# Performance work log

Measured on AMD Instinct MI355X. Metric: run time of the kernel, lower is better.

## Reference

```python
import jax, jax.numpy as jnp
import numpy as np

N = 100000   # points
C = 64       # in_planes
OUT = 64     # out_planes (== mid_planes)
S = 8        # share_planes
NS = 16      # nsample
EPS = 1e-5


def setup_inputs() -> dict:
    key = jax.random.key(0)
    ks = iter(jax.random.split(key, 40))
    rn = lambda shape, scale=1.0: jax.random.normal(next(ks), shape, jnp.float32) * scale

    inp = {
        'point': rn((N, 3)),
        'feat': rn((N, C)),
        'idx': jax.random.randint(next(ks), (N, NS), 0, N, jnp.int64),
        # linear_q / linear_k / linear_v
        'Wq': rn((C, OUT), C ** -0.5), 'bq': jnp.zeros((OUT,), jnp.float32),
        'Wk': rn((C, OUT), C ** -0.5), 'bk': jnp.zeros((OUT,), jnp.float32),
        'Wv': rn((C, OUT), C ** -0.5), 'bv': jnp.zeros((OUT,), jnp.float32),
        # linear_p: Dense(3) -> BN -> ReLU -> Dense(OUT)
        'p_W1': rn((3, 3), 3 ** -0.5), 'p_b1': rn((3,), 0.02),
        'p_g1': 1.0 + rn((3,), 0.02), 'p_be1': rn((3,), 0.02),
        'p_m1': rn((3,), 0.02), 'p_v1': 1.0 + 0.1 * jax.random.uniform(next(ks), (3,), jnp.float32),
        'p_W2': rn((3, OUT), 3 ** -0.5), 'p_b2': rn((OUT,), 0.02),
        # linear_w: BN -> ReLU -> Dense(OUT//S) -> BN -> ReLU -> Dense(OUT//S)
        'w_g1': 1.0 + rn((OUT,), 0.02), 'w_be1': rn((OUT,), 0.02),
        'w_m1': rn((OUT,), 0.02), 'w_v1': 1.0 + 0.1 * jax.random.uniform(next(ks), (OUT,), jnp.float32),
        'w_W1': rn((OUT, OUT // S), OUT ** -0.5), 'w_b1': rn((OUT // S,), 0.02),
        'w_g2': 1.0 + rn((OUT // S,), 0.02), 'w_be2': rn((OUT // S,), 0.02),
        'w_m2': rn((OUT // S,), 0.02), 'w_v2': 1.0 + 0.1 * jax.random.uniform(next(ks), (OUT // S,), jnp.float32),
        'w_W2': rn((OUT // S, OUT // S), (OUT // S) ** -0.5), 'w_b2': rn((OUT // S,), 0.02),
    }
    return inp


def _bn(x, g, b, m, v):  # inference-mode batchnorm over last axis
    return g * (x - m) * jax.lax.rsqrt(v + EPS) + b


def reference(point, feat, idx, Wq, bq, Wk, bk, Wv, bv,
              p_W1, p_b1, p_g1, p_be1, p_m1, p_v1, p_W2, p_b2,
              w_g1, w_be1, w_m1, w_v1, w_W1, w_b1,
              w_g2, w_be2, w_m2, w_v2, w_W2, w_b2):
    fq = feat @ Wq + bq                      # (n, out)
    fk = feat @ Wk + bk
    fv = feat @ Wv + bv

    # queryandgroup: KNN gather (idx precomputed)
    gx = point[idx] - point[:, None, :]      # (n, ns, 3) relative coords
    gk = fk[idx]                             # (n, ns, out)
    gv = fv[idx]                             # (n, ns, out)

    # linear_p position encoding MLP
    pr = jnp.maximum(_bn(gx @ p_W1 + p_b1, p_g1, p_be1, p_m1, p_v1), 0.0)
    pr = pr @ p_W2 + p_b2                    # (n, ns, out)

    # vector attention logits; out_planes//mid_planes == 1 so reduce_sum is identity
    w = gk - fq[:, None, :] + pr             # (n, ns, out)
    w = jnp.maximum(_bn(w, w_g1, w_be1, w_m1, w_v1), 0.0)
    w = w @ w_W1 + w_b1
    w = jnp.maximum(_bn(w, w_g2, w_be2, w_m2, w_v2), 0.0)
    w = w @ w_W2 + w_b2                      # (n, ns, out//s)
    w = jax.nn.softmax(w, axis=1)            # softmax over neighbors

    a = (gv + pr).reshape(-1, NS, S, OUT // S)         # (n, ns, s, out//s)
    out = jnp.sum(a * w[:, :, None, :], axis=1)        # (n, s, out//s)
    return out.reshape(-1, OUT)
```

## Files before the change

### kernel.cpp

```cpp
#include <hip/hip_runtime.h>
#include <hip/hip_fp16.h>

typedef unsigned short ushort_t;
typedef unsigned int u32;
typedef short short8 __attribute__((ext_vector_type(8)));
typedef float f32x2 __attribute__((ext_vector_type(2)));
typedef float f32x4 __attribute__((ext_vector_type(4)));
typedef u32 u32x4 __attribute__((ext_vector_type(4)));
typedef __fp16 h16x2 __attribute__((ext_vector_type(2)));
typedef _Float16 h16v8 __attribute__((ext_vector_type(8)));

#define N_PTS 100000
#define NSAMP 16
#define LOG2E 1.44269504088896340736f

__device__ __forceinline__ ushort_t f2h(float f) {
    __fp16 h = (__fp16)f; return __builtin_bit_cast(ushort_t, h);
}
__device__ __forceinline__ u32 pk2h(float lo, float hi) {
    return __builtin_bit_cast(u32, __builtin_amdgcn_cvt_pkrtz(lo, hi));
}
__device__ __forceinline__ float h2f_lo(u32 p) { return __low2float(__builtin_bit_cast(__half2, p)); }
__device__ __forceinline__ float h2f_hi(u32 p) { return __high2float(__builtin_bit_cast(__half2, p)); }
__device__ __forceinline__ u32 hadd2u(u32 a, u32 b) {
    return __builtin_bit_cast(u32, __hadd2(__builtin_bit_cast(__half2, a), __builtin_bit_cast(__half2, b)));
}
__device__ __forceinline__ u32 hsub2u(u32 a, u32 b) {
    return __builtin_bit_cast(u32, __hsub2(__builtin_bit_cast(__half2, a), __builtin_bit_cast(__half2, b)));
}
__device__ __forceinline__ u32 hmul2u(u32 a, u32 b) {
    return __builtin_bit_cast(u32, __hmul2(__builtin_bit_cast(__half2, a), __builtin_bit_cast(__half2, b)));
}
__device__ __forceinline__ u32 hmax2u(u32 a, u32 b) {
    u32 r; asm("v_pk_max_f16 %0, %1, %2" : "=v"(r) : "v"(a), "v"(b)); return r;
}
__device__ __forceinline__ float rfl(float x) {
    return __builtin_bit_cast(float, (int)__builtin_amdgcn_readfirstlane(__builtin_bit_cast(int, x)));
}
__device__ __forceinline__ f32x4 mfma16(u32x4 a, short8 b, f32x4 c) {
    return __builtin_amdgcn_mfma_f32_16x16x32_f16(
        __builtin_bit_cast(h16v8, a), __builtin_bit_cast(h16v8, b), c, 0, 0, 0);
}

__global__ __launch_bounds__(256, 4) void qkv_kernel(
    const float* __restrict__ feat,
    const float* __restrict__ Wq, const float* __restrict__ bq,
    const float* __restrict__ Wk, const float* __restrict__ bk,
    const float* __restrict__ Wv, const float* __restrict__ bv,
    ushort_t* __restrict__ qkv)
{
    const int tid  = threadIdx.x;
    const int lane = tid & 63;
    const int wid  = tid >> 6;
    const int jl   = lane & 15;
    const int g    = lane >> 4;

    const float* Ws[3] = {Wq, Wk, Wv};
    const float* bs[3] = {bq, bk, bv};

    short8 bfrag[3][4][2];
    float  bias[3][4];
#pragma unroll
    for (int m = 0; m < 3; m++)
#pragma unroll
        for (int cb = 0; cb < 4; cb++) {
#pragma unroll
            for (int h = 0; h < 2; h++) {
                short8 f;
#pragma unroll
                for (int e = 0; e < 8; e++)
                    f[e] = (short)f2h(Ws[m][(h * 32 + g * 8 + e) * 64 + cb * 16 + jl]);
                bfrag[m][cb][h] = f;
            }
            bias[m][cb] = bs[m][cb * 16 + jl];
        }

    const int nwaves = gridDim.x * (blockDim.x >> 6);
    const int gw     = blockIdx.x * (blockDim.x >> 6) + wid;
    const int ntiles = N_PTS / 16;

    for (int t = gw; t < ntiles; t += nwaves) {
        const int i0 = t * 16;
        const float* arow = feat + (i0 + jl) * 64;
        const f32x4 a00 = *(const f32x4*)(arow + g * 8);
        const f32x4 a01 = *(const f32x4*)(arow + g * 8 + 4);
        const f32x4 a10 = *(const f32x4*)(arow + 32 + g * 8);
        const f32x4 a11 = *(const f32x4*)(arow + 32 + g * 8 + 4);
        u32x4 ap0, ap1;
#pragma unroll
        for (int e = 0; e < 2; e++) {
            ap0[e]     = pk2h(a00[2 * e], a00[2 * e + 1]);
            ap0[2 + e] = pk2h(a01[2 * e], a01[2 * e + 1]);
            ap1[e]     = pk2h(a10[2 * e], a10[2 * e + 1]);
            ap1[2 + e] = pk2h(a11[2 * e], a11[2 * e + 1]);
        }
#pragma unroll
        for (int m = 0; m < 3; m++)
#pragma unroll
            for (int cb = 0; cb < 4; cb++) {
                f32x4 acc = {0.f, 0.f, 0.f, 0.f};
                acc = mfma16(ap0, bfrag[m][cb][0], acc);
                acc = mfma16(ap1, bfrag[m][cb][1], acc);
#pragma unroll
                for (int r = 0; r < 4; r++) {
                    const int row = i0 + g * 4 + r;
                    qkv[row * 192 + m * 64 + cb * 16 + jl] = f2h(acc[r] + bias[m][cb]);
                }
            }
    }
}

__global__ __launch_bounds__(256, 2) void attn_kernel(
    const float* __restrict__ point, const int* __restrict__ idx,
    const ushort_t* __restrict__ qkv,
    const float* pW1, const float* pb1, const float* pg1, const float* pbe1,
    const float* pm1, const float* pv1, const float* pW2, const float* pb2,
    const float* wg1, const float* wbe1, const float* wm1, const float* wv1,
    const float* wW1, const float* wb1, const float* wg2, const float* wbe2,
    const float* wm2, const float* wv2, const float* wW2, const float* wb2,
    float* __restrict__ out)
{
    __shared__ float lds[4][720];

    const int tid  = threadIdx.x;
    const int lane = tid & 63;
    const int wid  = tid >> 6;
    const int jl   = lane & 15;
    const int g    = lane >> 4;

    int zp = 0;
#pragma unroll
    for (int k = 0; k < 16; k++) zp |= idx[2 * k + 1];
    const bool idx64 = (zp == 0);

    float A1s[3][3], c1[3];
#pragma unroll
    for (int u = 0; u < 3; u++) {
        const float s = pg1[u] * rsqrtf(pv1[u] + 1e-5f);
        c1[u] = rfl((pb1[u] - pm1[u]) * s + pbe1[u]);
#pragma unroll
        for (int t = 0; t < 3; t++) A1s[t][u] = rfl(pW1[t * 3 + u] * s);
    }
    h16x2 w01[2][8];
    float w2c[2][8], pb2cc[2][8];
    u32 bwh[2][4];
#pragma unroll
    for (int h = 0; h < 2; h++) {
#pragma unroll
        for (int e = 0; e < 8; e++) {
            const int c = h * 32 + g * 8 + e;
            w01[h][e]   = __builtin_amdgcn_cvt_pkrtz(pW2[0 * 64 + c], pW2[1 * 64 + c]);
            w2c[h][e]   = pW2[2 * 64 + c];
            pb2cc[h][e] = pb2[c];
        }
#pragma unroll
        for (int q = 0; q < 4; q++) {
            const int c0 = h * 32 + g * 8 + 2 * q;
            const float s0 = wg1[c0] * rsqrtf(wv1[c0] + 1e-5f);
            const float s1 = wg1[c0 + 1] * rsqrtf(wv1[c0 + 1] + 1e-5f);
            bwh[h][q] = pk2h(wbe1[c0] / s0 - wm1[c0], wbe1[c0 + 1] / s1 - wm1[c0 + 1]);
        }
    }
    short8 w1f[2];
#pragma unroll
    for (int h = 0; h < 2; h++)
#pragma unroll
        for (int e = 0; e < 8; e++) {
            const int c = h * 32 + g * 8 + e;
            const float s = wg1[c] * rsqrtf(wv1[c] + 1e-5f);
            w1f[h][e] = (jl < 8) ? (short)f2h(wW1[c * 8 + jl] * s) : (short)0;
        }
    const float s2o  = (jl < 8) ? wg2[jl] * rsqrtf(wv2[jl] + 1e-5f) : 1.f;
    const float b2nd = (jl < 8) ? (wb1[jl] + wbe2[jl] / s2o - wm2[jl]) : 0.f;
    short8 w2f;
#pragma unroll
    for (int e = 0; e < 8; e++) {
        const float s2e = wg2[e] * rsqrtf(wv2[e] + 1e-5f);
        w2f[e] = (g == 0 && jl < 8) ? (short)f2h(wW2[e * 8 + jl] * s2e * LOG2E) : (short)0;
    }
    const float b2o = (jl < 8) ? wb2[jl] * LOG2E : 0.f;

    float* l12 = &lds[wid][0];
    u32*   tlu = (u32*)&lds[wid][192];

    const int nwaves = gridDim.x * (blockDim.x >> 6);
    const int gw     = blockIdx.x * (blockDim.x >> 6) + wid;

    const char* qb  = (const char*)qkv;
    const u32   gsl = (u32)g * 16u;

    for (int i = gw; i < N_PTS; i += nwaves) {
        const int nb = idx64 ? idx[(i * NSAMP + jl) * 2] : idx[i * NSAMP + jl];

        const u32 iOff = (u32)i * 384u + gsl;
        const u32 nOff = (u32)nb * 384u + gsl;

        const float px0 = point[i * 3 + 0];
        const float px1 = point[i * 3 + 1];
        const float px2 = point[i * 3 + 2];
        const float nx0 = point[nb * 3 + 0];
        const float nx1 = point[nb * 3 + 1];
        const float nx2 = point[nb * 3 + 2];
        const u32x4 fqp0 = *(const u32x4*)(qb + iOff);
        const u32x4 fqp1 = *(const u32x4*)(qb + iOff + 64);
        const u32x4 gkp0 = *(const u32x4*)(qb + nOff + 128);
        const u32x4 gkp1 = *(const u32x4*)(qb + nOff + 192);
        const u32x4 gvp0 = *(const u32x4*)(qb + nOff + 256);
        const u32x4 gvp1 = *(const u32x4*)(qb + nOff + 320);

        const float d0 = nx0 - px0, d1 = nx1 - px1, d2 = nx2 - px2;
        float y[3];
#pragma unroll
        for (int u = 0; u < 3; u++)
            y[u] = fmaxf(d0 * A1s[0][u] + d1 * A1s[1][u] + d2 * A1s[2][u] + c1[u], 0.f);
        const h16x2 y01h = __builtin_amdgcn_cvt_pkrtz(y[0], y[1]);
        u32 prp[2][4];
#pragma unroll
        for (int h = 0; h < 2; h++)
#pragma unroll
            for (int q = 0; q < 4; q++) {
                const float a0 = __builtin_amdgcn_fdot2(y01h, w01[h][2 * q],     pb2cc[h][2 * q],     false);
                const float a1 = __builtin_amdgcn_fdot2(y01h, w01[h][2 * q + 1], pb2cc[h][2 * q + 1], false);
                prp[h][q] = pk2h(fmaf(y[2], w2c[h][2 * q], a0), fmaf(y[2], w2c[h][2 * q + 1], a1));
            }

        u32x4 afp0, afp1;
#pragma unroll
        for (int q = 0; q < 4; q++) {
            const u32 pw0 = hadd2u(prp[0][q], bwh[0][q]);
            const u32 pw1 = hadd2u(prp[1][q], bwh[1][q]);
            afp0[q] = hmax2u(hadd2u(hsub2u(gkp0[q], fqp0[q]), pw0), 0u);
            afp1[q] = hmax2u(hadd2u(hsub2u(gkp1[q], fqp1[q]), pw1), 0u);
        }
        f32x4 u = {0.f, 0.f, 0.f, 0.f};
        u = mfma16(afp0, w1f[0], u);
        u = mfma16(afp1, w1f[1], u);

        if (jl < 8) {
#pragma unroll
            for (int r = 0; r < 4; r++)
                l12[(g * 4 + r) * 12 + jl] = fmaxf(u[r] + b2nd, 0.f);
        }
        __builtin_amdgcn_wave_barrier();
        u32x4 aU = {0u, 0u, 0u, 0u};
        if (g == 0) {
            const f32x4 ua = *(const f32x4*)(l12 + jl * 12);
            const f32x4 ub = *(const f32x4*)(l12 + jl * 12 + 4);
            aU[0] = pk2h(ua[0], ua[1]);
            aU[1] = pk2h(ua[2], ua[3]);
            aU[2] = pk2h(ub[0], ub[1]);
            aU[3] = pk2h(ub[2], ub[3]);
        }
        __builtin_amdgcn_wave_barrier();
        f32x4 u2 = {0.f, 0.f, 0.f, 0.f};
        u2 = mfma16(aU, w2f, u2);

        const float x0 = u2[0] + b2o, x1 = u2[1] + b2o, x2 = u2[2] + b2o, x3 = u2[3] + b2o;
        float m = fmaxf(fmaxf(x0, x1), fmaxf(x2, x3));
        m = fmaxf(m, __shfl_xor(m, 16, 64));
        m = fmaxf(m, __shfl_xor(m, 32, 64));
        const float e0 = exp2f(x0 - m), e1 = exp2f(x1 - m);
        const float e2 = exp2f(x2 - m), e3 = exp2f(x3 - m);
        float ssum = e0 + e1 + e2 + e3;
        ssum += __shfl_xor(ssum, 16, 64);
        ssum += __shfl_xor(ssum, 32, 64);
        const float inv = 1.0f / ssum;

        if (jl < 8) {
            l12[(g * 4 + 0) * 12 + jl] = e0 * inv;
            l12[(g * 4 + 1) * 12 + jl] = e1 * inv;
            l12[(g * 4 + 2) * 12 + jl] = e2 * inv;
            l12[(g * 4 + 3) * 12 + jl] = e3 * inv;
        }
        __builtin_amdgcn_wave_barrier();
        const f32x4 wa  = *(const f32x4*)(l12 + jl * 12);
        const f32x4 wbv = *(const f32x4*)(l12 + jl * 12 + 4);
        __builtin_amdgcn_wave_barrier();
        u32 wh[4];
        wh[0] = pk2h(wa[0], wa[1]);
        wh[1] = pk2h(wa[2], wa[3]);
        wh[2] = pk2h(wbv[0], wbv[1]);
        wh[3] = pk2h(wbv[2], wbv[3]);

        u32* trow = tlu + jl * 33 + g * 4;
#pragma unroll
        for (int q = 0; q < 4; q++) {
            trow[q]      = hmul2u(hadd2u(gvp0[q], prp[0][q]), wh[q]);
            trow[16 + q] = hmul2u(hadd2u(gvp1[q], prp[1][q]), wh[q]);
        }
        __builtin_amdgcn_wave_barrier();

        if (lane < 32) {
            const u32* tb = tlu + lane;
            u32 v[16];
#pragma unroll
            for (int j = 0; j < 16; j++) v[j] = tb[j * 33];
#pragma unroll
            for (int s = 8; s >= 1; s >>= 1)
#pragma unroll
                for (int j = 0; j < 16; j++)
                    if (j < s) v[j] = hadd2u(v[j], v[j + s]);
            f32x2 o;
            o[0] = h2f_lo(v[0]);
            o[1] = h2f_hi(v[0]);
            *(f32x2*)(out + i * 64 + 2 * lane) = o;
        }
    }
}

extern "C" void kernel_launch(void* const* d_in, const int* in_sizes, int n_in,
                              void* d_out, int out_size, void* d_ws, size_t ws_size,
                              hipStream_t stream) {
    const float* point = (const float*)d_in[0];
    const float* feat  = (const float*)d_in[1];
    const int*   idx   = (const int*)d_in[2];
    const float* Wq = (const float*)d_in[3];  const float* bq = (const float*)d_in[4];
    const float* Wk = (const float*)d_in[5];  const float* bk = (const float*)d_in[6];
    const float* Wv = (const float*)d_in[7];  const float* bv = (const float*)d_in[8];
    const float* pW1  = (const float*)d_in[9];
    const float* pb1  = (const float*)d_in[10];
    const float* pg1  = (const float*)d_in[11];
    const float* pbe1 = (const float*)d_in[12];
    const float* pm1  = (const float*)d_in[13];
    const float* pv1  = (const float*)d_in[14];
    const float* pW2  = (const float*)d_in[15];
    const float* pb2  = (const float*)d_in[16];
    const float* wg1  = (const float*)d_in[17];
    const float* wbe1 = (const float*)d_in[18];
    const float* wm1  = (const float*)d_in[19];
    const float* wv1  = (const float*)d_in[20];
    const float* wW1  = (const float*)d_in[21];
    const float* wb1  = (const float*)d_in[22];
    const float* wg2  = (const float*)d_in[23];
    const float* wbe2 = (const float*)d_in[24];
    const float* wm2  = (const float*)d_in[25];
    const float* wv2  = (const float*)d_in[26];
    const float* wW2  = (const float*)d_in[27];
    const float* wb2  = (const float*)d_in[28];

    ushort_t* qkv  = (ushort_t*)d_ws;
    float*    outp = (float*)d_out;

    hipLaunchKernelGGL(qkv_kernel, dim3(512), dim3(256), 0, stream,
                       feat, Wq, bq, Wk, bk, Wv, bv, qkv);
    hipLaunchKernelGGL(attn_kernel, dim3(2048), dim3(256), 0, stream,
                       point, idx, qkv,
                       pW1, pb1, pg1, pbe1, pm1, pv1, pW2, pb2,
                       wg1, wbe1, wm1, wv1, wW1, wb1,
                       wg2, wbe2, wm2, wv2, wW2, wb2,
                       outp);
}
```

Before: 128.4 us.

## Use single-wave blocks and split neighbor reduction across full wave

Changes the attention kernel from 256-thread blocks with four waves sharing LDS to 64-thread single-wave blocks (8192 blocks), each with its own small LDS region. The final 16-row neighbor reduction is now split so both half-waves each sum 8 rows and combine with a cross-lane shuffle, instead of only 32 lanes doing all 16 loads. The LDS transpose stride changes from 33 to 34 so stores can be 64-bit vector writes. Smaller blocks may improve scheduling granularity, but the per-block parameter setup is repeated more often and the padding change may alter bank conflicts.

```diff
diff --git a/kernel.cpp b/kernel.cpp
--- a/kernel.cpp
+++ b/kernel.cpp
@@ -6,6 +6,7 @@
 typedef short short8 __attribute__((ext_vector_type(8)));
 typedef float f32x2 __attribute__((ext_vector_type(2)));
 typedef float f32x4 __attribute__((ext_vector_type(4)));
+typedef u32 u32x2 __attribute__((ext_vector_type(2)));
 typedef u32 u32x4 __attribute__((ext_vector_type(4)));
 typedef __fp16 h16x2 __attribute__((ext_vector_type(2)));
 typedef _Float16 h16v8 __attribute__((ext_vector_type(8)));
@@ -110,7 +111,7 @@
     }
 }
 
-__global__ __launch_bounds__(256, 2) void attn_kernel(
+__global__ __launch_bounds__(64, 2) void attn_kernel(
     const float* __restrict__ point, const int* __restrict__ idx,
     const ushort_t* __restrict__ qkv,
     const float* pW1, const float* pb1, const float* pg1, const float* pbe1,
@@ -120,11 +121,9 @@
     const float* wm2, const float* wv2, const float* wW2, const float* wb2,
     float* __restrict__ out)
 {
-    __shared__ float lds[4][720];
-
-    const int tid  = threadIdx.x;
-    const int lane = tid & 63;
-    const int wid  = tid >> 6;
+    __shared__ float lds[736];
+
+    const int lane = threadIdx.x & 63;
     const int jl   = lane & 15;
     const int g    = lane >> 4;
 
@@ -180,11 +179,11 @@
     }
     const float b2o = (jl < 8) ? wb2[jl] * LOG2E : 0.f;
 
-    float* l12 = &lds[wid][0];
-    u32*   tlu = (u32*)&lds[wid][192];
-
-    const int nwaves = gridDim.x * (blockDim.x >> 6);
-    const int gw     = blockIdx.x * (blockDim.x >> 6) + wid;
+    float* l12 = &lds[0];
+    u32*   tlu = (u32*)&lds[192];
+
+    const int nwaves = gridDim.x;
+    const int gw     = blockIdx.x;
 
     const char* qb  = (const char*)qkv;
     const u32   gsl = (u32)g * 16u;
@@ -282,27 +281,37 @@
         wh[2] = pk2h(wbv[0], wbv[1]);
         wh[3] = pk2h(wbv[2], wbv[3]);
 
-        u32* trow = tlu + jl * 33 + g * 4;
-#pragma unroll
-        for (int q = 0; q < 4; q++) {
-            trow[q]      = hmul2u(hadd2u(gvp0[q], prp[0][q]), wh[q]);
-            trow[16 + q] = hmul2u(hadd2u(gvp1[q], prp[1][q]), wh[q]);
-        }
-        __builtin_amdgcn_wave_barrier();
-
+        u32* trow = tlu + jl * 34 + g * 4;
+        u32x2 p00, p01, p10, p11;
+        p00[0] = hmul2u(hadd2u(gvp0[0], prp[0][0]), wh[0]);
+        p00[1] = hmul2u(hadd2u(gvp0[1], prp[0][1]), wh[1]);
+        p01[0] = hmul2u(hadd2u(gvp0[2], prp[0][2]), wh[2]);
+        p01[1] = hmul2u(hadd2u(gvp0[3], prp[0][3]), wh[3]);
+        p10[0] = hmul2u(hadd2u(gvp1[0], prp[1][0]), wh[0]);
+        p10[1] = hmul2u(hadd2u(gvp1[1], prp[1][1]), wh[1]);
+        p11[0] = hmul2u(hadd2u(gvp1[2], prp[1][2]), wh[2]);
+        p11[1] = hmul2u(hadd2u(gvp1[3], prp[1][3]), wh[3]);
+        *(u32x2*)(trow + 0)  = p00;
+        *(u32x2*)(trow + 2)  = p01;
+        *(u32x2*)(trow + 16) = p10;
+        *(u32x2*)(trow + 18) = p11;
+        __builtin_amdgcn_wave_barrier();
+
+        const u32* tb = tlu + (lane & 31);
+        const int rbase = (lane >> 5) * 8;
+        u32 v[8];
+#pragma unroll
+        for (int j = 0; j < 8; j++) v[j] = tb[(rbase + j) * 34];
+#pragma unroll
+        for (int s = 4; s >= 1; s >>= 1)
+#pragma unroll
+            for (int j = 0; j < s; j++) v[j] = hadd2u(v[j], v[j + s]);
+        const u32 o32 = (u32)__shfl_xor((int)v[0], 32, 64);
+        const u32 tot = hadd2u(v[0], o32);
         if (lane < 32) {
-            const u32* tb = tlu + lane;
-            u32 v[16];
-#pragma unroll
-            for (int j = 0; j < 16; j++) v[j] = tb[j * 33];
-#pragma unroll
-            for (int s = 8; s >= 1; s >>= 1)
-#pragma unroll
-                for (int j = 0; j < 16; j++)
-                    if (j < s) v[j] = hadd2u(v[j], v[j + s]);
             f32x2 o;
-            o[0] = h2f_lo(v[0]);
-            o[1] = h2f_hi(v[0]);
+            o[0] = h2f_lo(tot);
+            o[1] = h2f_hi(tot);
             *(f32x2*)(out + i * 64 + 2 * lane) = o;
         }
     }
@@ -343,7 +352,7 @@
 
     hipLaunchKernelGGL(qkv_kernel, dim3(512), dim3(256), 0, stream,
                        feat, Wq, bq, Wk, bk, Wv, bv, qkv);
-    hipLaunchKernelGGL(attn_kernel, dim3(2048), dim3(256), 0, stream,
+    hipLaunchKernelGGL(attn_kernel, dim3(8192), dim3(64), 0, stream,
                        point, idx, qkv,
                        pW1, pb1, pg1, pbe1, pm1, pv1, pW2, pb2,
                        wg1, wbe1, wm1, wv1, wW1, wb1,
```

New measurement: 124.3 us. 3.2% less time.
